# Optimization experiments

Hardware: AMD Instinct MI355X
Metric: run time of the kernel (lower is better)

Reference implementation:

```python
import jax, jax.numpy as jnp
import numpy as np

B, CIN, H, W = 32, 192, 56, 56
COUT, K, PAD, STRIDE = 192, 3, 1, 1


def setup_inputs() -> dict:
    key = jax.random.key(0)
    k1, k2 = jax.random.split(key, 2)
    x = jax.random.normal(k1, (B, CIN, H, W), dtype=jnp.float32)
    # torch Linear: weight [out_feature, in_feature*k*k], bias [out_feature]
    weight = jax.random.normal(k2, (COUT, CIN * K * K), dtype=jnp.float32) * 0.02
    bias = jnp.zeros((COUT,), dtype=jnp.float32)
    return {"x": x, "weight": weight, "bias": bias}


def reference(x, weight, bias):
    # pad H/W with zeros (F.pad constant)
    xp = jnp.pad(x, ((0, 0), (0, 0), (PAD, PAD), (PAD, PAD)))
    Bn, C, Hp, Wp = xp.shape
    Ho = (Hp - K) // STRIDE + 1
    Wo = (Wp - K) // STRIDE + 1
    # im2col matching torch.nn.Unfold layout: feature index = c*K*K + i*K + j
    # small fixed loop over K*K kernel offsets (9 slices), fully vectorized over B,C,Ho,Wo
    patches = jnp.stack(
        [xp[:, :, i : i + Ho * STRIDE : STRIDE, j : j + Wo * STRIDE : STRIDE]
         for i in range(K) for j in range(K)],
        axis=2,
    )  # [B, C, K*K, Ho, Wo]
    cols = patches.reshape(Bn, C * K * K, Ho * Wo)  # [B, C*K*K, L]
    # Linear over transposed unfold: out[b, l, o] = cols[b, :, l] @ weight[o, :].T + bias
    out = jnp.einsum('bkl,ok->bol', cols, weight) + bias[None, :, None]
    # rearrange 'b (h w) c -> b c h w' with h=w=sqrt(L)
    return out.reshape(Bn, COUT, Ho, Wo)
```

## Files before the change

kernel.cpp:

```cpp
#include <hip/hip_runtime.h>

typedef __attribute__((ext_vector_type(8))) short short8;
typedef __attribute__((ext_vector_type(4))) float floatx4;

#define CIN    192
#define COUTN  192
#define HWDIM  56
#define HWSZ   (56*56)
#define KWT    1728
#define PH     58
#define CK     32
#define NCHUNK 6

#define XPACK_SHORTS (32u*6u*58u*58u*32u)
#define WPACK_SHORTS (3u*6u*9u*64u*32u)
#define WS_NEEDED    ((size_t)(XPACK_SHORTS + WPACK_SHORTS) * 2u)

__device__ __forceinline__ short f2bf(float f) {
    union { float f; unsigned u; } v; v.f = f;
    unsigned u = v.u + 0x7FFFu + ((v.u >> 16) & 1u);
    return (short)(u >> 16);
}

__global__ __launch_bounds__(256)
void pack_x(const float* __restrict__ x, short* __restrict__ xp) {
    const int hq = blockIdx.x;
    const int cc = blockIdx.y;
    const int b  = blockIdx.z;
    const int tid = threadIdx.x;
    short* dst = xp + ((size_t)((b * 6 + cc) * 58 + hq) * 58) * CK;

    if (hq == 0 || hq == 57) {
        if (tid < 232) *(short8*)(dst + tid * 8) = (short8){0,0,0,0,0,0,0,0};
        return;
    }

    __shared__ unsigned lds[56 * 20];
    const int h = hq - 1;

    if (tid < 224) {
        int cpair = tid / 14, f4 = tid % 14;
        const float* s1 = x + ((size_t)(b * CIN + cc * 32 + cpair * 2) * HWSZ) + h * 56 + f4 * 4;
        floatx4 v1 = *(const floatx4*)s1;
        floatx4 v2 = *(const floatx4*)(s1 + HWSZ);
#pragma unroll
        for (int k = 0; k < 4; ++k) {
            unsigned pr = (unsigned short)f2bf(v1[k]) | ((unsigned)(unsigned short)f2bf(v2[k]) << 16);
            lds[(f4 * 4 + k) * 20 + cpair] = pr;
        }
    }
    __syncthreads();
    if (tid < 232) {
        int xq = tid >> 2, q = tid & 3;
        short8 v = (short8){0,0,0,0,0,0,0,0};
        if (xq >= 1 && xq <= 56)
            v = *(const short8*)&lds[(xq - 1) * 20 + q * 4];
        *(short8*)(dst + tid * 8) = v;
    }
}

__global__ __launch_bounds__(256)
void pack_w(const float* __restrict__ w, short* __restrict__ wp) {
    int idx = blockIdx.x * 256 + threadIdx.x;
    const int TOT = 3 * 6 * 9 * 64 * 4;
    if (idx >= TOT) return;
    int cg = idx & 3;
    int m  = (idx >> 2) & 63;
    int t  = idx >> 8;
    int off = t % 9;  t /= 9;
    int cc  = t % 6;
    int og  = t / 6;
    short8 v;
#pragma unroll
    for (int k = 0; k < 8; ++k)
        v[k] = f2bf(w[(size_t)(og * 64 + m) * KWT + (cc * 32 + cg * 8 + k) * 9 + off]);
    *(short8*)(wp + (size_t)idx * 8) = v;
}

__global__ __launch_bounds__(256, 2)
void conv_main(const short* __restrict__ xp, const short* __restrict__ wp,
               const float* __restrict__ bias, float* __restrict__ out) {
    __shared__ __align__(16) short sh[10 * PH * CK];

    const int tid  = threadIdx.x;
    const int gh0  = blockIdx.x * 8;
    const int og   = blockIdx.y;
    const int bb   = blockIdx.z;
    const int lane = tid & 63;
    const int wave = tid >> 6;
    const int g    = lane >> 4;
    const int col  = lane & 15;

    int pb[7];
#pragma unroll
    for (int nt = 0; nt < 7; ++nt) {
        int l = wave * 112 + nt * 16 + col;
        pb[nt] = (l / 56) * PH + (l % 56);
    }

    floatx4 acc[4][7];
#pragma unroll
    for (int mt = 0; mt < 4; ++mt)
#pragma unroll
        for (int nt = 0; nt < 7; ++nt)
            acc[mt][nt] = (floatx4){0.f, 0.f, 0.f, 0.f};

    const short8* wpk = (const short8*)wp;

    for (int cc = 0; cc < NCHUNK; ++cc) {
        if (cc) __syncthreads();

        const short* src = xp + ((size_t)(bb * 6 + cc) * (PH * PH) + (size_t)gh0 * PH) * CK;
#pragma unroll
        for (int j = 0; j < 10; ++j) {
            int idx = j * 256 + tid;
            if (idx < 2320) {
                int p  = idx >> 2, sg = idx & 3;
                int gc = (p << 2) | (sg ^ ((p >> 1) & 3));
                __builtin_amdgcn_global_load_lds(
                    (const __attribute__((address_space(1))) void*)(src + (size_t)gc * 8),
                    (__attribute__((address_space(3))) void*)(sh + (j * 256 + wave * 64) * 8),
                    16, 0, 0);
            }
        }
        __syncthreads();

        const int wb = (og * 6 + cc) * 9 * 256;
#pragma unroll
        for (int off = 0; off < 9; ++off) {
            const int di = off / 3, dj = off % 3;
            short8 afr[4];
#pragma unroll
            for (int mt = 0; mt < 4; ++mt)
                afr[mt] = wpk[wb + off * 256 + (mt * 16 + col) * 4 + g];
#pragma unroll
            for (int nt = 0; nt < 7; ++nt) {
                int p  = pb[nt] + di * PH + dj;
                int ch = (p << 2) | (g ^ ((p >> 1) & 3));
                short8 bfr = *(const short8*)&sh[ch * 8];
                acc[0][nt] = __builtin_amdgcn_mfma_f32_16x16x32_bf16(afr[0], bfr, acc[0][nt], 0, 0, 0);
                acc[1][nt] = __builtin_amdgcn_mfma_f32_16x16x32_bf16(afr[1], bfr, acc[1][nt], 0, 0, 0);
                acc[2][nt] = __builtin_amdgcn_mfma_f32_16x16x32_bf16(afr[2], bfr, acc[2][nt], 0, 0, 0);
                acc[3][nt] = __builtin_amdgcn_mfma_f32_16x16x32_bf16(afr[3], bfr, acc[3][nt], 0, 0, 0);
            }
        }
    }

#pragma unroll
    for (int mt = 0; mt < 4; ++mt) {
        int o = og * 64 + mt * 16 + g * 4;
        float b0 = bias[o], b1 = bias[o + 1], b2 = bias[o + 2], b3 = bias[o + 3];
#pragma unroll
        for (int nt = 0; nt < 7; ++nt) {
            int l  = wave * 112 + nt * 16 + col;
            int h  = gh0 + l / 56;
            int ww = l % 56;
            size_t base = ((size_t)(bb * COUTN + o) * HWDIM + h) * HWDIM + ww;
            floatx4 v = acc[mt][nt];
            out[base]                     = v[0] + b0;
            out[base + (size_t)HWSZ]      = v[1] + b1;
            out[base + (size_t)2 * HWSZ]  = v[2] + b2;
            out[base + (size_t)3 * HWSZ]  = v[3] + b3;
        }
    }
}

__global__ __launch_bounds__(256, 2)
void conv3x3_fb(const float* __restrict__ x, const float* __restrict__ w,
                const float* __restrict__ bias, float* __restrict__ out) {
    __shared__ __align__(16) short sh_halo[6 * 58 * 32];
    __shared__ __align__(16) short sh_w[9 * 64 * 32];
    const int tid = threadIdx.x;
    const int gh0 = blockIdx.x * 4;
    const int o0  = blockIdx.y * 64;
    const int bb  = blockIdx.z;
    const int lane = tid & 63, wave = tid >> 6;
    const int wm = wave >> 1, wn = wave & 1;
    const int g = lane >> 4, col = lane & 15;
    int ly[7], lx[7];
#pragma unroll
    for (int nt = 0; nt < 7; ++nt) {
        int l = wn * 112 + nt * 16 + col;
        ly[nt] = l / 56; lx[nt] = l % 56;
    }
    floatx4 acc[2][7];
#pragma unroll
    for (int mt = 0; mt < 2; ++mt)
#pragma unroll
        for (int nt = 0; nt < 7; ++nt) acc[mt][nt] = (floatx4){0.f,0.f,0.f,0.f};
    for (int cc = 0; cc < NCHUNK; ++cc) {
        const int c0 = cc * 32;
        if (cc) __syncthreads();
        for (int i = tid; i < 4 * 6 * 58; i += 256) {
            int xx = i % 58, r = i / 58, y = r % 6, cg = r / 6;
            int gh = gh0 + y - 1, gw = xx - 1;
            bool ok = ((unsigned)gh < 56u) & ((unsigned)gw < 56u);
            const float* src = x + ((size_t)(bb * CIN + c0 + cg * 8) * HWDIM + gh) * HWDIM + gw;
            short8 v;
#pragma unroll
            for (int k = 0; k < 8; ++k) v[k] = f2bf(ok ? src[k * HWSZ] : 0.f);
            *(short8*)&sh_halo[(y * 58 + xx) * 32 + ((cg ^ ((xx >> 1) & 3)) << 3)] = v;
        }
        for (int i = tid; i < 9 * 64 * 4; i += 256) {
            int cg = i & 3, off = (i >> 2) % 9, m = i / 36;
            const float* src = w + (size_t)(o0 + m) * KWT + (c0 + cg * 8) * 9 + off;
            short8 v;
#pragma unroll
            for (int k = 0; k < 8; ++k) v[k] = f2bf(src[k * 9]);
            *(short8*)&sh_w[(off * 64 + m) * 32 + ((cg ^ ((m >> 1) & 3)) << 3)] = v;
        }
        __syncthreads();
#pragma unroll
        for (int off = 0; off < 9; ++off) {
            const int di = off / 3, dj = off % 3;
            short8 a[2];
#pragma unroll
            for (int mt = 0; mt < 2; ++mt) {
                int m = wm * 32 + mt * 16 + col;
                a[mt] = *(const short8*)&sh_w[(off * 64 + m) * 32 + ((g ^ ((m >> 1) & 3)) << 3)];
            }
#pragma unroll
            for (int nt = 0; nt < 7; ++nt) {
                int yy = ly[nt] + di, xpp = lx[nt] + dj;
                short8 bfr = *(const short8*)&sh_halo[(yy * 58 + xpp) * 32 + ((g ^ ((xpp >> 1) & 3)) << 3)];
                acc[0][nt] = __builtin_amdgcn_mfma_f32_16x16x32_bf16(a[0], bfr, acc[0][nt], 0, 0, 0);
                acc[1][nt] = __builtin_amdgcn_mfma_f32_16x16x32_bf16(a[1], bfr, acc[1][nt], 0, 0, 0);
            }
        }
    }
#pragma unroll
    for (int mt = 0; mt < 2; ++mt) {
        int o = o0 + wm * 32 + mt * 16 + g * 4;
#pragma unroll
        for (int nt = 0; nt < 7; ++nt) {
            int l = wn * 112 + nt * 16 + col;
            int h = gh0 + l / 56, ww = l % 56;
            size_t base = ((size_t)(bb * COUTN + o) * HWDIM + h) * HWDIM + ww;
            floatx4 v = acc[mt][nt];
#pragma unroll
            for (int r2 = 0; r2 < 4; ++r2)
                out[base + (size_t)r2 * HWSZ] = v[r2] + bias[o + r2];
        }
    }
}

extern "C" void kernel_launch(void* const* d_in, const int* in_sizes, int n_in,
                              void* d_out, int out_size, void* d_ws, size_t ws_size,
                              hipStream_t stream) {
    const float* x  = (const float*)d_in[0];
    const float* wt = (const float*)d_in[1];
    const float* bi = (const float*)d_in[2];
    float* out = (float*)d_out;

    if (ws_size >= WS_NEEDED) {
        short* xpk = (short*)d_ws;
        short* wpk = xpk + XPACK_SHORTS;
        pack_x<<<dim3(58, 6, 32), 256, 0, stream>>>(x, xpk);
        {
            int tot = 3 * 6 * 9 * 64 * 4;
            pack_w<<<(tot + 255) / 256, 256, 0, stream>>>(wt, wpk);
        }
        conv_main<<<dim3(7, 3, 32), dim3(256), 0, stream>>>(xpk, wpk, bi, out);
    } else {
        conv3x3_fb<<<dim3(14, 3, 32), dim3(256), 0, stream>>>(x, wt, bi, out);
    }
}
```

Baseline: 224.4 us.

## Fuse input bf16 packing into conv kernel covering all output channels

Removes the separate pack_x pass, which wrote a padded bf16 copy of the input to workspace. The conv kernel now reads fp32 input directly, converts it to bf16 and stages it into LDS with the swizzle. Each 512-thread block now covers all 192 output channels over 4 rows, so every input tile is loaded once instead of three times, and the weight fragments for the next offset are prefetched. The cost is strided scalar fp32 gathers (8 channels per slot at stride HWSZ) instead of 16-byte async loads, plus per-block conversion work and a different occupancy and register profile.

New measurement: 334.8 us. 49.2% more time.

```diff
diff --git a/kernel.cpp b/kernel.cpp
--- a/kernel.cpp
+++ b/kernel.cpp
@@ -9,12 +9,10 @@
 #define HWSZ   (56*56)
 #define KWT    1728
 #define PH     58
-#define CK     32
 #define NCHUNK 6
 
-#define XPACK_SHORTS (32u*6u*58u*58u*32u)
-#define WPACK_SHORTS (3u*6u*9u*64u*32u)
-#define WS_NEEDED    ((size_t)(XPACK_SHORTS + WPACK_SHORTS) * 2u)
+#define WPACK_SHORTS (6u*9u*192u*32u)
+#define WS_NEEDED    ((size_t)WPACK_SHORTS * 2u)
 
 __device__ __forceinline__ short f2bf(float f) {
     union { float f; unsigned u; } v; v.f = f;
@@ -23,144 +21,120 @@
 }
 
 __global__ __launch_bounds__(256)
-void pack_x(const float* __restrict__ x, short* __restrict__ xp) {
-    const int hq = blockIdx.x;
-    const int cc = blockIdx.y;
-    const int b  = blockIdx.z;
-    const int tid = threadIdx.x;
-    short* dst = xp + ((size_t)((b * 6 + cc) * 58 + hq) * 58) * CK;
-
-    if (hq == 0 || hq == 57) {
-        if (tid < 232) *(short8*)(dst + tid * 8) = (short8){0,0,0,0,0,0,0,0};
-        return;
-    }
-
-    __shared__ unsigned lds[56 * 20];
-    const int h = hq - 1;
-
-    if (tid < 224) {
-        int cpair = tid / 14, f4 = tid % 14;
-        const float* s1 = x + ((size_t)(b * CIN + cc * 32 + cpair * 2) * HWSZ) + h * 56 + f4 * 4;
-        floatx4 v1 = *(const floatx4*)s1;
-        floatx4 v2 = *(const floatx4*)(s1 + HWSZ);
-#pragma unroll
-        for (int k = 0; k < 4; ++k) {
-            unsigned pr = (unsigned short)f2bf(v1[k]) | ((unsigned)(unsigned short)f2bf(v2[k]) << 16);
-            lds[(f4 * 4 + k) * 20 + cpair] = pr;
-        }
-    }
-    __syncthreads();
-    if (tid < 232) {
-        int xq = tid >> 2, q = tid & 3;
-        short8 v = (short8){0,0,0,0,0,0,0,0};
-        if (xq >= 1 && xq <= 56)
-            v = *(const short8*)&lds[(xq - 1) * 20 + q * 4];
-        *(short8*)(dst + tid * 8) = v;
-    }
-}
-
-__global__ __launch_bounds__(256)
 void pack_w(const float* __restrict__ w, short* __restrict__ wp) {
     int idx = blockIdx.x * 256 + threadIdx.x;
-    const int TOT = 3 * 6 * 9 * 64 * 4;
+    const int TOT = 6 * 9 * 192 * 4;
     if (idx >= TOT) return;
     int cg = idx & 3;
-    int m  = (idx >> 2) & 63;
-    int t  = idx >> 8;
-    int off = t % 9;  t /= 9;
-    int cc  = t % 6;
-    int og  = t / 6;
+    int m  = (idx >> 2) % 192;
+    int t  = idx / (4 * 192);
+    int off = t % 9;
+    int cc  = t / 9;
     short8 v;
 #pragma unroll
     for (int k = 0; k < 8; ++k)
-        v[k] = f2bf(w[(size_t)(og * 64 + m) * KWT + (cc * 32 + cg * 8 + k) * 9 + off]);
+        v[k] = f2bf(w[(size_t)m * KWT + (cc * 32 + cg * 8 + k) * 9 + off]);
     *(short8*)(wp + (size_t)idx * 8) = v;
 }
 
-__global__ __launch_bounds__(256, 2)
-void conv_main(const short* __restrict__ xp, const short* __restrict__ wp,
-               const float* __restrict__ bias, float* __restrict__ out) {
-    __shared__ __align__(16) short sh[10 * PH * CK];
+__global__ __launch_bounds__(512, 4)
+void conv_fused(const float* __restrict__ x, const short* __restrict__ wp,
+                const float* __restrict__ bias, float* __restrict__ out) {
+    __shared__ __align__(16) short sh[6 * PH * 32];
 
     const int tid  = threadIdx.x;
-    const int gh0  = blockIdx.x * 8;
-    const int og   = blockIdx.y;
-    const int bb   = blockIdx.z;
+    const int gh0  = blockIdx.x * 4;
+    const int bb   = blockIdx.y;
     const int lane = tid & 63;
     const int wave = tid >> 6;
+    const int wm   = wave >> 1;
+    const int wn   = wave & 1;
     const int g    = lane >> 4;
     const int col  = lane & 15;
 
     int pb[7];
 #pragma unroll
     for (int nt = 0; nt < 7; ++nt) {
-        int l = wave * 112 + nt * 16 + col;
+        int l = wn * 112 + nt * 16 + col;
         pb[nt] = (l / 56) * PH + (l % 56);
     }
 
-    floatx4 acc[4][7];
-#pragma unroll
-    for (int mt = 0; mt < 4; ++mt)
+    floatx4 acc[3][7];
+#pragma unroll
+    for (int mt = 0; mt < 3; ++mt)
 #pragma unroll
         for (int nt = 0; nt < 7; ++nt)
             acc[mt][nt] = (floatx4){0.f, 0.f, 0.f, 0.f};
 
     const short8* wpk = (const short8*)wp;
+    const int mchunk = (wm * 48 + col) * 4 + g;
 
     for (int cc = 0; cc < NCHUNK; ++cc) {
         if (cc) __syncthreads();
 
-        const short* src = xp + ((size_t)(bb * 6 + cc) * (PH * PH) + (size_t)gh0 * PH) * CK;
-#pragma unroll
-        for (int j = 0; j < 10; ++j) {
-            int idx = j * 256 + tid;
-            if (idx < 2320) {
-                int p  = idx >> 2, sg = idx & 3;
-                int gc = (p << 2) | (sg ^ ((p >> 1) & 3));
-                __builtin_amdgcn_global_load_lds(
-                    (const __attribute__((address_space(1))) void*)(src + (size_t)gc * 8),
-                    (__attribute__((address_space(3))) void*)(sh + (j * 256 + wave * 64) * 8),
-                    16, 0, 0);
+#pragma unroll
+        for (int it = 0; it < 3; ++it) {
+            int slot = it * 512 + tid;
+            if (slot < 1392) {
+                int xx = slot % 58;
+                int t  = slot / 58;
+                int y  = t % 6;
+                int cg = t / 6;
+                int gh = gh0 + y - 1;
+                int gw = xx - 1;
+                short8 v = (short8){0, 0, 0, 0, 0, 0, 0, 0};
+                if (((unsigned)gh < 56u) & ((unsigned)gw < 56u)) {
+                    const float* src = x + ((size_t)(bb * CIN + cc * 32 + cg * 8) * HWSZ) + gh * HWDIM + gw;
+#pragma unroll
+                    for (int k = 0; k < 8; ++k) v[k] = f2bf(src[(size_t)k * HWSZ]);
+                }
+                int p = y * PH + xx;
+                *(short8*)&sh[(((p << 2) | (cg ^ ((p >> 1) & 3))) << 3)] = v;
             }
         }
         __syncthreads();
 
-        const int wb = (og * 6 + cc) * 9 * 256;
+        const int wb = cc * 9;
+        short8 afr[3], nafr[3];
+#pragma unroll
+        for (int mt = 0; mt < 3; ++mt)
+            afr[mt] = wpk[(size_t)wb * 768 + mchunk + mt * 64];
 #pragma unroll
         for (int off = 0; off < 9; ++off) {
             const int di = off / 3, dj = off % 3;
-            short8 afr[4];
-#pragma unroll
-            for (int mt = 0; mt < 4; ++mt)
-                afr[mt] = wpk[wb + off * 256 + (mt * 16 + col) * 4 + g];
+            if (off < 8) {
+#pragma unroll
+                for (int mt = 0; mt < 3; ++mt)
+                    nafr[mt] = wpk[(size_t)(wb + off + 1) * 768 + mchunk + mt * 64];
+            }
 #pragma unroll
             for (int nt = 0; nt < 7; ++nt) {
-                int p  = pb[nt] + di * PH + dj;
-                int ch = (p << 2) | (g ^ ((p >> 1) & 3));
-                short8 bfr = *(const short8*)&sh[ch * 8];
+                int p = pb[nt] + di * PH + dj;
+                short8 bfr = *(const short8*)&sh[(((p << 2) | (g ^ ((p >> 1) & 3))) << 3)];
                 acc[0][nt] = __builtin_amdgcn_mfma_f32_16x16x32_bf16(afr[0], bfr, acc[0][nt], 0, 0, 0);
                 acc[1][nt] = __builtin_amdgcn_mfma_f32_16x16x32_bf16(afr[1], bfr, acc[1][nt], 0, 0, 0);
                 acc[2][nt] = __builtin_amdgcn_mfma_f32_16x16x32_bf16(afr[2], bfr, acc[2][nt], 0, 0, 0);
-                acc[3][nt] = __builtin_amdgcn_mfma_f32_16x16x32_bf16(afr[3], bfr, acc[3][nt], 0, 0, 0);
-            }
-        }
-    }
-
-#pragma unroll
-    for (int mt = 0; mt < 4; ++mt) {
-        int o = og * 64 + mt * 16 + g * 4;
+            }
+#pragma unroll
+            for (int mt = 0; mt < 3; ++mt) afr[mt] = nafr[mt];
+        }
+    }
+
+#pragma unroll
+    for (int mt = 0; mt < 3; ++mt) {
+        int o = wm * 48 + mt * 16 + g * 4;
         float b0 = bias[o], b1 = bias[o + 1], b2 = bias[o + 2], b3 = bias[o + 3];
 #pragma unroll
         for (int nt = 0; nt < 7; ++nt) {
-            int l  = wave * 112 + nt * 16 + col;
+            int l  = wn * 112 + nt * 16 + col;
             int h  = gh0 + l / 56;
             int ww = l % 56;
             size_t base = ((size_t)(bb * COUTN + o) * HWDIM + h) * HWDIM + ww;
             floatx4 v = acc[mt][nt];
-            out[base]                     = v[0] + b0;
-            out[base + (size_t)HWSZ]      = v[1] + b1;
-            out[base + (size_t)2 * HWSZ]  = v[2] + b2;
-            out[base + (size_t)3 * HWSZ]  = v[3] + b3;
+            out[base]                    = v[0] + b0;
+            out[base + (size_t)HWSZ]     = v[1] + b1;
+            out[base + (size_t)2 * HWSZ] = v[2] + b2;
+            out[base + (size_t)3 * HWSZ] = v[3] + b3;
         }
     }
 }
@@ -253,14 +227,10 @@
     float* out = (float*)d_out;
 
     if (ws_size >= WS_NEEDED) {
-        short* xpk = (short*)d_ws;
-        short* wpk = xpk + XPACK_SHORTS;
-        pack_x<<<dim3(58, 6, 32), 256, 0, stream>>>(x, xpk);
-        {
-            int tot = 3 * 6 * 9 * 64 * 4;
-            pack_w<<<(tot + 255) / 256, 256, 0, stream>>>(wt, wpk);
-        }
-        conv_main<<<dim3(7, 3, 32), dim3(256), 0, stream>>>(xpk, wpk, bi, out);
+        short* wpk = (short*)d_ws;
+        int tot = 6 * 9 * 192 * 4;
+        pack_w<<<(tot + 255) / 256, 256, 0, stream>>>(wt, wpk);
+        conv_fused<<<dim3(14, 32), dim3(512), 0, stream>>>(x, wpk, bi, out);
     } else {
         conv3x3_fb<<<dim3(14, 3, 32), dim3(256), 0, stream>>>(x, wt, bi, out);
     }
```
